# Kernel optimization log

Measured on AMD Instinct MI355X. Metric: run time of the kernel, lower is better.

Reference implementation:

```python
import jax, jax.numpy as jnp
import numpy as np
import math

C_IN = 1024
C = 64
N_HEAD = 16
B, S = 4, 1024


def setup_inputs() -> dict:
    key = jax.random.key(0)
    ks = jax.random.split(key, 8)
    scale = 1.0 / math.sqrt(C_IN)
    x = jax.random.normal(ks[0], (B, S, C_IN), dtype=jnp.float32)
    bias = jax.random.normal(ks[1], (B, N_HEAD, S, S), dtype=jnp.float32) * 0.1
    attention_mask = jax.random.randint(ks[2], (B, S), 0, 2, dtype=jnp.int32)
    Wq = jax.random.normal(ks[3], (C_IN, C * N_HEAD), dtype=jnp.float32) * scale
    Wk = jax.random.normal(ks[4], (C_IN, C * N_HEAD), dtype=jnp.float32) * scale
    Wv = jax.random.normal(ks[5], (C_IN, C * N_HEAD), dtype=jnp.float32) * scale
    Wo = jax.random.normal(ks[6], (C * N_HEAD, C_IN), dtype=jnp.float32) * scale
    bo = jax.random.normal(ks[7], (C_IN,), dtype=jnp.float32) * 0.01
    return {"x": x, "bias": bias, "attention_mask": attention_mask,
            "Wq": Wq, "Wk": Wk, "Wv": Wv, "Wo": Wo, "bo": bo}


def reference(x, bias, attention_mask, Wq, Wk, Wv, Wo, bo):
    # x: (B, S, c_in); attn_dim=1 so the attention axis is already at -2.
    q = x @ Wq  # (B, S, H*c)
    k = x @ Wk
    v = x @ Wv
    # split heads: (B, S, H, c) -> (B, H, S, c)
    def split_heads(t):
        return t.reshape(t.shape[:-1] + (N_HEAD, C)).swapaxes(-2, -3)
    q, k, v = split_heads(q), split_heads(k), split_heads(v)
    q = q / math.sqrt(C)
    a = jnp.einsum('bhqc,bhkc->bhqk', q, k)  # (B, H, S, S)
    a = a + bias
    offset = jnp.where(attention_mask[:, None, None, :] == 0, -1e8, 0.0).astype(a.dtype)
    a = a + offset
    a = jax.nn.softmax(a, axis=-1)
    o = jnp.einsum('bhqk,bhkc->bhqc', a, v)  # (B, H, S, c)
    o = o.swapaxes(-3, -2).reshape(B, S, N_HEAD * C)
    out = o @ Wo + bo  # (B, S, c_in)
    return out
```

## Files before the change

kernel.cpp:

```cpp
#include <hip/hip_runtime.h>
#include <hip/hip_bf16.h>
#include <math.h>

#define B_   4
#define S_   1024
#define CIN  1024
#define H_   16
#define CH   64
#define HC   1024

typedef __bf16 bf16;
typedef __bf16 bf16x8 __attribute__((ext_vector_type(8)));
typedef __bf16 bf16x4 __attribute__((ext_vector_type(4)));
typedef float  f32x4  __attribute__((ext_vector_type(4)));

__device__ __forceinline__ void gld16(const bf16* g, bf16* l) {
  __builtin_amdgcn_global_load_lds(
      (const __attribute__((address_space(1))) unsigned int*)g,
      (__attribute__((address_space(3))) unsigned int*)l,
      16, 0, 0);
}

__global__ __launch_bounds__(256) void cast_x_kernel(const float* __restrict__ x,
                                                     bf16* __restrict__ xb) {
  int i = (blockIdx.x * 256 + threadIdx.x) * 4;
  f32x4 v = *(const f32x4*)(x + i);
  bf16x4 o;
  o[0] = (bf16)v[0]; o[1] = (bf16)v[1]; o[2] = (bf16)v[2]; o[3] = (bf16)v[3];
  *(bf16x4*)(xb + i) = o;
}

__global__ __launch_bounds__(256) void transW_kernel(
    const float* __restrict__ Wq, const float* __restrict__ Wk,
    const float* __restrict__ Wv, const float* __restrict__ Wo,
    bf16* __restrict__ Wqkvt, bf16* __restrict__ Wot) {
  const float* W; bf16* Wt;
  switch (blockIdx.z) {
    case 0: W = Wq; Wt = Wqkvt; break;
    case 1: W = Wk; Wt = Wqkvt + (size_t)1024 * 1024; break;
    case 2: W = Wv; Wt = Wqkvt + (size_t)2048 * 1024; break;
    default: W = Wo; Wt = Wot; break;
  }
  __shared__ float tile[64][65];
  const int r0 = blockIdx.y * 64, c0 = blockIdx.x * 64;
  const int tx = threadIdx.x & 63, ty = threadIdx.x >> 6;
#pragma unroll
  for (int j = 0; j < 64; j += 4)
    tile[ty + j][tx] = W[(size_t)(r0 + ty + j) * 1024 + c0 + tx];
  __syncthreads();
#pragma unroll
  for (int j = 0; j < 64; j += 4)
    Wt[(size_t)(c0 + ty + j) * 1024 + r0 + tx] = (bf16)tile[tx][ty + j];
}

template <int MODE>
__global__ __launch_bounds__(256) void gemm_kernel(
    const bf16* __restrict__ A, const bf16* __restrict__ Bt,
    bf16* __restrict__ Qa, bf16* __restrict__ Ka, bf16* __restrict__ Vt,
    float* __restrict__ outf, const float* __restrict__ bo) {
  __shared__ bf16 Asm[128 * 32];
  __shared__ bf16 Bsm[128 * 32];
  const int tid = threadIdx.x;
  const int lane = tid & 63, wave = tid >> 6;
  const int m0 = blockIdx.y * 128, n0 = blockIdx.x * 128;
  const int wr = wave >> 1, wc = wave & 1;
  const int K = 1024;

  f32x4 acc[4][4] = {};

  const int srow = tid >> 2;
  const int scol = (tid & 3) * 8;
  const size_t abase = (size_t)(m0 + srow) * K + scol;
  const size_t bbase = (size_t)(n0 + srow) * K + scol;
  bf16* lA = Asm + wave * 512;
  bf16* lB = Bsm + wave * 512;

  for (int kt = 0; kt < K; kt += 32) {
    gld16(A + abase + kt, lA);
    gld16(A + abase + (size_t)64 * K + kt, lA + 2048);
    gld16(Bt + bbase + kt, lB);
    gld16(Bt + bbase + (size_t)64 * K + kt, lB + 2048);
    __syncthreads();
    bf16x8 af[4], bfr[4];
#pragma unroll
    for (int m = 0; m < 4; m++)
      af[m] = *(const bf16x8*)(Asm + (wr * 64 + m * 16 + (lane & 15)) * 32 + (lane >> 4) * 8);
#pragma unroll
    for (int n = 0; n < 4; n++)
      bfr[n] = *(const bf16x8*)(Bsm + (wc * 64 + n * 16 + (lane & 15)) * 32 + (lane >> 4) * 8);
    __builtin_amdgcn_s_setprio(1);
#pragma unroll
    for (int m = 0; m < 4; m++)
#pragma unroll
      for (int n = 0; n < 4; n++)
        acc[m][n] = __builtin_amdgcn_mfma_f32_16x16x32_bf16(af[m], bfr[n], acc[m][n], 0, 0, 0);
    __builtin_amdgcn_s_setprio(0);
    __syncthreads();
  }

#pragma unroll
  for (int m = 0; m < 4; m++) {
#pragma unroll
    for (int n = 0; n < 4; n++) {
      const int col = n0 + wc * 64 + n * 16 + (lane & 15);
      const int grow = m0 + wr * 64 + m * 16 + (lane >> 4) * 4;
      if (MODE == 0) {
        const int which = col >> 10;
        const int hcol = col & 1023, hh = hcol >> 6, cc = hcol & 63;
        const int bb = grow >> 10, s0v = grow & 1023;
        if (which == 0) {
          const size_t base = (((size_t)bb * H_ + hh) * S_ + s0v) * CH + cc;
#pragma unroll
          for (int r = 0; r < 4; r++)
            Qa[base + (size_t)r * CH] = (bf16)(acc[m][n][r] * 0.125f);
        } else if (which == 1) {
          const size_t base = (((size_t)bb * H_ + hh) * S_ + s0v) * CH + cc;
#pragma unroll
          for (int r = 0; r < 4; r++)
            Ka[base + (size_t)r * CH] = (bf16)acc[m][n][r];
        } else {
          bf16x4 pv;
#pragma unroll
          for (int r = 0; r < 4; r++) pv[r] = (bf16)acc[m][n][r];
          *(bf16x4*)(Vt + (((size_t)bb * H_ + hh) * CH + cc) * S_ + s0v) = pv;
        }
      } else {
        const float bv = bo[col];
#pragma unroll
        for (int r = 0; r < 4; r++)
          outf[(size_t)(grow + r) * 1024 + col] = acc[m][n][r] + bv;
      }
    }
  }
}

__global__ __launch_bounds__(256) void attn_kernel(
    const bf16* __restrict__ Q, const bf16* __restrict__ Ka,
    const bf16* __restrict__ Vt, const float* __restrict__ bias,
    const int* __restrict__ mask, bf16* __restrict__ O) {
  const int bh = blockIdx.y, b = bh >> 4, h = bh & 15;
  const int q0 = blockIdx.x * 64;
  const int tid = threadIdx.x, wave = tid >> 6, lane = tid & 63;
  const int qr = lane & 15, kg = lane >> 4;

  __shared__ bf16 Ksm[64][72];
  __shared__ bf16 Vsm[64][72];
  __shared__ bf16 Psm[4][16][72];
  __shared__ float Bsm[64][68];
  __shared__ float Msm[S_];

  {
    const int4 mv = *(const int4*)(mask + (size_t)b * S_ + tid * 4);
    f32x4 mo;
    mo[0] = (mv.x == 0) ? -1e8f : 0.f;
    mo[1] = (mv.y == 0) ? -1e8f : 0.f;
    mo[2] = (mv.z == 0) ? -1e8f : 0.f;
    mo[3] = (mv.w == 0) ? -1e8f : 0.f;
    *(f32x4*)(Msm + tid * 4) = mo;
  }

  const bf16* Qp = Q + ((size_t)bh * S_ + q0 + wave * 16 + qr) * CH;
  bf16x8 qf[2];
  qf[0] = *(const bf16x8*)(Qp + kg * 8);
  qf[1] = *(const bf16x8*)(Qp + 32 + kg * 8);

  f32x4 oacc[4] = {};
  float mrow[4] = {-1e30f, -1e30f, -1e30f, -1e30f};
  float lrow[4] = {0.f, 0.f, 0.f, 0.f};

  const bf16* Kp = Ka + (size_t)bh * S_ * CH;
  const bf16* Vp = Vt + (size_t)bh * CH * S_;
  const float* biasT = bias + ((size_t)bh * S_ + q0) * S_;

  const int srow = tid >> 2, scol = (tid & 3) * 16;
  const int brow = tid >> 4, bcol = (tid & 15) * 4;

  bf16x8 kr0, kr1, vr0, vr1;
  f32x4 brg[4];

  {
    const int k0 = 0;
    kr0 = *(const bf16x8*)(Kp + (size_t)(k0 + srow) * CH + scol);
    kr1 = *(const bf16x8*)(Kp + (size_t)(k0 + srow) * CH + scol + 8);
    vr0 = *(const bf16x8*)(Vp + (size_t)srow * S_ + k0 + scol);
    vr1 = *(const bf16x8*)(Vp + (size_t)srow * S_ + k0 + scol + 8);
#pragma unroll
    for (int i = 0; i < 4; i++)
      brg[i] = *(const f32x4*)(biasT + (size_t)(brow + i * 16) * S_ + k0 + bcol);
  }

  for (int t = 0; t < S_ / 64; t++) {
    const int k0 = t * 64;
    __syncthreads();
    *(bf16x8*)&Ksm[srow][scol] = kr0;
    *(bf16x8*)&Ksm[srow][scol + 8] = kr1;
    *(bf16x8*)&Vsm[srow][scol] = vr0;
    *(bf16x8*)&Vsm[srow][scol + 8] = vr1;
#pragma unroll
    for (int i = 0; i < 4; i++)
      *(f32x4*)&Bsm[brow + i * 16][bcol] = brg[i];
    if (t + 1 < S_ / 64) {
      const int kn = k0 + 64;
      kr0 = *(const bf16x8*)(Kp + (size_t)(kn + srow) * CH + scol);
      kr1 = *(const bf16x8*)(Kp + (size_t)(kn + srow) * CH + scol + 8);
      vr0 = *(const bf16x8*)(Vp + (size_t)srow * S_ + kn + scol);
      vr1 = *(const bf16x8*)(Vp + (size_t)srow * S_ + kn + scol + 8);
#pragma unroll
      for (int i = 0; i < 4; i++)
        brg[i] = *(const f32x4*)(biasT + (size_t)(brow + i * 16) * S_ + kn + bcol);
    }
    __syncthreads();

    f32x4 sf[4] = {};
    __builtin_amdgcn_s_setprio(1);
#pragma unroll
    for (int n = 0; n < 4; n++) {
#pragma unroll
      for (int j = 0; j < 2; j++) {
        bf16x8 kf = *(const bf16x8*)&Ksm[n * 16 + qr][j * 32 + kg * 8];
        sf[n] = __builtin_amdgcn_mfma_f32_16x16x32_bf16(qf[j], kf, sf[n], 0, 0, 0);
      }
    }
    __builtin_amdgcn_s_setprio(0);
#pragma unroll
    for (int n = 0; n < 4; n++) {
      const float moff = Msm[k0 + n * 16 + qr];
#pragma unroll
      for (int r = 0; r < 4; r++)
        sf[n][r] += Bsm[wave * 16 + kg * 4 + r][n * 16 + qr] + moff;
    }
#pragma unroll
    for (int r = 0; r < 4; r++) {
      float tm = fmaxf(fmaxf(sf[0][r], sf[1][r]), fmaxf(sf[2][r], sf[3][r]));
      tm = fmaxf(tm, __shfl_xor(tm, 1));
      tm = fmaxf(tm, __shfl_xor(tm, 2));
      tm = fmaxf(tm, __shfl_xor(tm, 4));
      tm = fmaxf(tm, __shfl_xor(tm, 8));
      const float nm = fmaxf(mrow[r], tm);
      const float al = __expf(mrow[r] - nm);
      mrow[r] = nm;
      float rs = 0.f;
#pragma unroll
      for (int n = 0; n < 4; n++) {
        const float p = __expf(sf[n][r] - nm);
        sf[n][r] = p;
        rs += p;
      }
      rs += __shfl_xor(rs, 1);
      rs += __shfl_xor(rs, 2);
      rs += __shfl_xor(rs, 4);
      rs += __shfl_xor(rs, 8);
      lrow[r] = lrow[r] * al + rs;
#pragma unroll
      for (int n = 0; n < 4; n++) oacc[n][r] *= al;
    }
#pragma unroll
    for (int n = 0; n < 4; n++)
#pragma unroll
      for (int r = 0; r < 4; r++)
        Psm[wave][kg * 4 + r][n * 16 + qr] = (bf16)sf[n][r];
    __asm__ volatile("s_waitcnt lgkmcnt(0)" ::: "memory");
    __builtin_amdgcn_s_setprio(1);
#pragma unroll
    for (int n = 0; n < 4; n++) {
#pragma unroll
      for (int j = 0; j < 2; j++) {
        bf16x8 pf = *(const bf16x8*)&Psm[wave][qr][j * 32 + kg * 8];
        bf16x8 vf = *(const bf16x8*)&Vsm[n * 16 + qr][j * 32 + kg * 8];
        oacc[n] = __builtin_amdgcn_mfma_f32_16x16x32_bf16(pf, vf, oacc[n], 0, 0, 0);
      }
    }
    __builtin_amdgcn_s_setprio(0);
  }
#pragma unroll
  for (int r = 0; r < 4; r++) {
    const float inv = 1.0f / lrow[r];
    const int s = q0 + wave * 16 + kg * 4 + r;
#pragma unroll
    for (int n = 0; n < 4; n++)
      O[((size_t)b * S_ + s) * HC + h * CH + n * 16 + qr] = (bf16)(oacc[n][r] * inv);
  }
}

extern "C" void kernel_launch(void* const* d_in, const int* in_sizes, int n_in,
                              void* d_out, int out_size, void* d_ws, size_t ws_size,
                              hipStream_t stream) {
  (void)in_sizes; (void)n_in; (void)out_size; (void)ws_size;
  const float* x    = (const float*)d_in[0];
  const float* bias = (const float*)d_in[1];
  const int*   mask = (const int*)d_in[2];
  const float* Wq   = (const float*)d_in[3];
  const float* Wk   = (const float*)d_in[4];
  const float* Wv   = (const float*)d_in[5];
  const float* Wo   = (const float*)d_in[6];
  const float* bo   = (const float*)d_in[7];
  float* out = (float*)d_out;

  char* ws = (char*)d_ws;
  bf16* xb    = (bf16*)(ws);
  bf16* Wqkvt = (bf16*)(ws + (8u  << 20));
  bf16* Wot   = (bf16*)(ws + (14u << 20));
  bf16* Qa    = (bf16*)(ws + (16u << 20));
  bf16* Kaa   = (bf16*)(ws + (24u << 20));
  bf16* Vtr   = (bf16*)(ws + (32u << 20));
  bf16* Oa    = (bf16*)(ws + (40u << 20));

  cast_x_kernel<<<4096, 256, 0, stream>>>(x, xb);
  transW_kernel<<<dim3(16, 16, 4), 256, 0, stream>>>(Wq, Wk, Wv, Wo, Wqkvt, Wot);
  gemm_kernel<0><<<dim3(24, 32), 256, 0, stream>>>(xb, Wqkvt, Qa, Kaa, Vtr, nullptr, nullptr);
  attn_kernel<<<dim3(16, 64), 256, 0, stream>>>(Qa, Kaa, Vtr, bias, mask, Oa);
  gemm_kernel<1><<<dim3(8, 32), 256, 0, stream>>>(Oa, Wot, nullptr, nullptr, nullptr, out, bo);
}
```

Measured before the change: 489.7 us.

## Load K/V/bias fragments directly from global, drop shared staging and barriers

```diff
diff --git a/kernel.cpp b/kernel.cpp
--- a/kernel.cpp
+++ b/kernel.cpp
@@ -141,12 +141,9 @@
   const int bh = blockIdx.y, b = bh >> 4, h = bh & 15;
   const int q0 = blockIdx.x * 64;
   const int tid = threadIdx.x, wave = tid >> 6, lane = tid & 63;
-  const int qr = lane & 15, kg = lane >> 4;
-
-  __shared__ bf16 Ksm[64][72];
-  __shared__ bf16 Vsm[64][72];
+  const int l15 = lane & 15, kg = lane >> 4;
+
   __shared__ bf16 Psm[4][16][72];
-  __shared__ float Bsm[64][68];
   __shared__ float Msm[S_];
 
   {
@@ -158,127 +155,115 @@
     mo[3] = (mv.w == 0) ? -1e8f : 0.f;
     *(f32x4*)(Msm + tid * 4) = mo;
   }
-
-  const bf16* Qp = Q + ((size_t)bh * S_ + q0 + wave * 16 + qr) * CH;
-  bf16x8 qf[2];
-  qf[0] = *(const bf16x8*)(Qp + kg * 8);
-  qf[1] = *(const bf16x8*)(Qp + 32 + kg * 8);
+  __syncthreads();
+
+  const int qrow = q0 + wave * 16 + l15;
+  const bf16* Qp = Q + ((size_t)bh * S_ + qrow) * CH;
+  const bf16x8 qf0 = *(const bf16x8*)(Qp + kg * 8);
+  const bf16x8 qf1 = *(const bf16x8*)(Qp + 32 + kg * 8);
+
+  const bf16*  Kp = Ka + (size_t)bh * S_ * CH + kg * 8;
+  const bf16*  Vp = Vt + ((size_t)bh * CH + l15) * S_ + kg * 8;
+  const float* bp = bias + ((size_t)bh * S_ + qrow) * S_ + kg * 4;
 
   f32x4 oacc[4] = {};
-  float mrow[4] = {-1e30f, -1e30f, -1e30f, -1e30f};
-  float lrow[4] = {0.f, 0.f, 0.f, 0.f};
-
-  const bf16* Kp = Ka + (size_t)bh * S_ * CH;
-  const bf16* Vp = Vt + (size_t)bh * CH * S_;
-  const float* biasT = bias + ((size_t)bh * S_ + q0) * S_;
-
-  const int srow = tid >> 2, scol = (tid & 3) * 16;
-  const int brow = tid >> 4, bcol = (tid & 15) * 4;
-
-  bf16x8 kr0, kr1, vr0, vr1;
-  f32x4 brg[4];
-
-  {
-    const int k0 = 0;
-    kr0 = *(const bf16x8*)(Kp + (size_t)(k0 + srow) * CH + scol);
-    kr1 = *(const bf16x8*)(Kp + (size_t)(k0 + srow) * CH + scol + 8);
-    vr0 = *(const bf16x8*)(Vp + (size_t)srow * S_ + k0 + scol);
-    vr1 = *(const bf16x8*)(Vp + (size_t)srow * S_ + k0 + scol + 8);
-#pragma unroll
-    for (int i = 0; i < 4; i++)
-      brg[i] = *(const f32x4*)(biasT + (size_t)(brow + i * 16) * S_ + k0 + bcol);
-  }
-
-  for (int t = 0; t < S_ / 64; t++) {
-    const int k0 = t * 64;
-    __syncthreads();
-    *(bf16x8*)&Ksm[srow][scol] = kr0;
-    *(bf16x8*)&Ksm[srow][scol + 8] = kr1;
-    *(bf16x8*)&Vsm[srow][scol] = vr0;
-    *(bf16x8*)&Vsm[srow][scol + 8] = vr1;
-#pragma unroll
-    for (int i = 0; i < 4; i++)
-      *(f32x4*)&Bsm[brow + i * 16][bcol] = brg[i];
-    if (t + 1 < S_ / 64) {
-      const int kn = k0 + 64;
-      kr0 = *(const bf16x8*)(Kp + (size_t)(kn + srow) * CH + scol);
-      kr1 = *(const bf16x8*)(Kp + (size_t)(kn + srow) * CH + scol + 8);
-      vr0 = *(const bf16x8*)(Vp + (size_t)srow * S_ + kn + scol);
-      vr1 = *(const bf16x8*)(Vp + (size_t)srow * S_ + kn + scol + 8);
-#pragma unroll
-      for (int i = 0; i < 4; i++)
-        brg[i] = *(const f32x4*)(biasT + (size_t)(brow + i * 16) * S_ + kn + bcol);
-    }
-    __syncthreads();
+  float mrow = -1e30f, lrow = 0.f;
+
+#pragma unroll 1
+  for (int k0 = 0; k0 < S_; k0 += 64) {
+    f32x4 brg[4];
+#pragma unroll
+    for (int m = 0; m < 4; m++)
+      brg[m] = *(const f32x4*)(bp + k0 + m * 16);
+    bf16x8 kf[4][2];
+#pragma unroll
+    for (int m = 0; m < 4; m++) {
+      const bf16* kr = Kp + (size_t)(k0 + m * 16 + l15) * CH;
+      kf[m][0] = *(const bf16x8*)(kr);
+      kf[m][1] = *(const bf16x8*)(kr + 32);
+    }
+    bf16x8 vf[4][2];
+#pragma unroll
+    for (int n = 0; n < 4; n++) {
+      const bf16* vr = Vp + (size_t)(n * 16) * S_ + k0;
+      vf[n][0] = *(const bf16x8*)(vr);
+      vf[n][1] = *(const bf16x8*)(vr + 32);
+    }
 
     f32x4 sf[4] = {};
     __builtin_amdgcn_s_setprio(1);
 #pragma unroll
-    for (int n = 0; n < 4; n++) {
-#pragma unroll
-      for (int j = 0; j < 2; j++) {
-        bf16x8 kf = *(const bf16x8*)&Ksm[n * 16 + qr][j * 32 + kg * 8];
-        sf[n] = __builtin_amdgcn_mfma_f32_16x16x32_bf16(qf[j], kf, sf[n], 0, 0, 0);
-      }
+    for (int m = 0; m < 4; m++) {
+      sf[m] = __builtin_amdgcn_mfma_f32_16x16x32_bf16(kf[m][0], qf0, sf[m], 0, 0, 0);
+      sf[m] = __builtin_amdgcn_mfma_f32_16x16x32_bf16(kf[m][1], qf1, sf[m], 0, 0, 0);
     }
     __builtin_amdgcn_s_setprio(0);
-#pragma unroll
-    for (int n = 0; n < 4; n++) {
-      const float moff = Msm[k0 + n * 16 + qr];
-#pragma unroll
-      for (int r = 0; r < 4; r++)
-        sf[n][r] += Bsm[wave * 16 + kg * 4 + r][n * 16 + qr] + moff;
-    }
-#pragma unroll
-    for (int r = 0; r < 4; r++) {
-      float tm = fmaxf(fmaxf(sf[0][r], sf[1][r]), fmaxf(sf[2][r], sf[3][r]));
-      tm = fmaxf(tm, __shfl_xor(tm, 1));
-      tm = fmaxf(tm, __shfl_xor(tm, 2));
-      tm = fmaxf(tm, __shfl_xor(tm, 4));
-      tm = fmaxf(tm, __shfl_xor(tm, 8));
-      const float nm = fmaxf(mrow[r], tm);
-      const float al = __expf(mrow[r] - nm);
-      mrow[r] = nm;
-      float rs = 0.f;
-#pragma unroll
-      for (int n = 0; n < 4; n++) {
-        const float p = __expf(sf[n][r] - nm);
-        sf[n][r] = p;
+
+#pragma unroll
+    for (int m = 0; m < 4; m++) {
+      const f32x4 mo = *(const f32x4*)(Msm + k0 + m * 16 + kg * 4);
+      sf[m] = sf[m] + brg[m] + mo;
+    }
+
+    float tm = fmaxf(fmaxf(fmaxf(sf[0][0], sf[0][1]), fmaxf(sf[0][2], sf[0][3])),
+                     fmaxf(fmaxf(sf[1][0], sf[1][1]), fmaxf(sf[1][2], sf[1][3])));
+    tm = fmaxf(tm, fmaxf(fmaxf(fmaxf(sf[2][0], sf[2][1]), fmaxf(sf[2][2], sf[2][3])),
+                         fmaxf(fmaxf(sf[3][0], sf[3][1]), fmaxf(sf[3][2], sf[3][3]))));
+    tm = fmaxf(tm, __shfl_xor(tm, 16));
+    tm = fmaxf(tm, __shfl_xor(tm, 32));
+    const float nm = fmaxf(mrow, tm);
+    const float al = __expf(mrow - nm);
+    mrow = nm;
+    float rs = 0.f;
+#pragma unroll
+    for (int m = 0; m < 4; m++)
+#pragma unroll
+      for (int r = 0; r < 4; r++) {
+        const float p = __expf(sf[m][r] - nm);
+        sf[m][r] = p;
         rs += p;
       }
-      rs += __shfl_xor(rs, 1);
-      rs += __shfl_xor(rs, 2);
-      rs += __shfl_xor(rs, 4);
-      rs += __shfl_xor(rs, 8);
-      lrow[r] = lrow[r] * al + rs;
-#pragma unroll
-      for (int n = 0; n < 4; n++) oacc[n][r] *= al;
-    }
+    rs += __shfl_xor(rs, 16);
+    rs += __shfl_xor(rs, 32);
+    lrow = lrow * al + rs;
+
+#pragma unroll
+    for (int m = 0; m < 4; m++) {
+      bf16x4 pv;
+#pragma unroll
+      for (int r = 0; r < 4; r++) pv[r] = (bf16)sf[m][r];
+      *(bf16x4*)&Psm[wave][l15][m * 16 + kg * 4] = pv;
+    }
+
+    f32x4 av;
+#pragma unroll
+    for (int r = 0; r < 4; r++) av[r] = __shfl(al, (lane & 48) | (kg * 4 + r));
+#pragma unroll
+    for (int n = 0; n < 4; n++) oacc[n] *= av;
+
+    __asm__ volatile("s_waitcnt lgkmcnt(0)" ::: "memory");
+    const bf16x8 pf0 = *(const bf16x8*)&Psm[wave][l15][kg * 8];
+    const bf16x8 pf1 = *(const bf16x8*)&Psm[wave][l15][32 + kg * 8];
+
+    __builtin_amdgcn_s_setprio(1);
+#pragma unroll
+    for (int n = 0; n < 4; n++) {
+      oacc[n] = __builtin_amdgcn_mfma_f32_16x16x32_bf16(pf0, vf[n][0], oacc[n], 0, 0, 0);
+      oacc[n] = __builtin_amdgcn_mfma_f32_16x16x32_bf16(pf1, vf[n][1], oacc[n], 0, 0, 0);
+    }
+    __builtin_amdgcn_s_setprio(0);
+  }
+
+  f32x4 inv4;
+#pragma unroll
+  for (int r = 0; r < 4; r++)
+    inv4[r] = 1.0f / __shfl(lrow, (lane & 48) | (kg * 4 + r));
+#pragma unroll
+  for (int r = 0; r < 4; r++) {
+    const int s = q0 + wave * 16 + kg * 4 + r;
 #pragma unroll
     for (int n = 0; n < 4; n++)
-#pragma unroll
-      for (int r = 0; r < 4; r++)
-        Psm[wave][kg * 4 + r][n * 16 + qr] = (bf16)sf[n][r];
-    __asm__ volatile("s_waitcnt lgkmcnt(0)" ::: "memory");
-    __builtin_amdgcn_s_setprio(1);
-#pragma unroll
-    for (int n = 0; n < 4; n++) {
-#pragma unroll
-      for (int j = 0; j < 2; j++) {
-        bf16x8 pf = *(const bf16x8*)&Psm[wave][qr][j * 32 + kg * 8];
-        bf16x8 vf = *(const bf16x8*)&Vsm[n * 16 + qr][j * 32 + kg * 8];
-        oacc[n] = __builtin_amdgcn_mfma_f32_16x16x32_bf16(pf, vf, oacc[n], 0, 0, 0);
-      }
-    }
-    __builtin_amdgcn_s_setprio(0);
-  }
-#pragma unroll
-  for (int r = 0; r < 4; r++) {
-    const float inv = 1.0f / lrow[r];
-    const int s = q0 + wave * 16 + kg * 4 + r;
-#pragma unroll
-    for (int n = 0; n < 4; n++)
-      O[((size_t)b * S_ + s) * HC + h * CH + n * 16 + qr] = (bf16)(oacc[n][r] * inv);
+      O[((size_t)b * S_ + s) * HC + h * CH + n * 16 + l15] = (bf16)(oacc[n][r] * inv4[r]);
   }
 }
 
```

Result: slower. 520.5 us (+6.3%).
